# Optimization experiments

Hardware: AMD Instinct MI355X
Metric: run time of the kernel (lower is better)

## Reference

```python
import jax, jax.numpy as jnp
import numpy as np

N = 50000   # nodes
E = 800000  # edges (avg degree 16)
H = 128     # h_dim
S = 64      # s_dim
HID = 128   # master_selection_hidden_dim
K = 500     # num master nodes = master_rate(0.01) * N
LAM = 0.5   # lambda_attn


def setup_inputs() -> dict:
    key = jax.random.key(0)
    ks = jax.random.split(key, 24)
    rn = lambda k, shp, s: jax.random.normal(k, shp, dtype=jnp.float32) * s
    return {
        "h": rn(ks[0], (N, H), 1.0),
        "h_global": rn(ks[1], (N, H), 1.0),
        "pos": rn(ks[2], (N, 3), 1.0),
        "edge_index": jax.random.randint(ks[3], (2, E), 0, N, dtype=jnp.int32),
        "batch": jnp.zeros((N,), dtype=jnp.int32),
        "W_a": rn(ks[4], (H, H), H ** -0.5),
        "W_b": rn(ks[5], (H, H), H ** -0.5),
        "b1": rn(ks[6], (H,), 0.02),
        "W2": rn(ks[7], (H, H), H ** -0.5),
        "b2": rn(ks[8], (H,), 0.02),
        "W3": rn(ks[9], (2 * H, H), (2 * H) ** -0.5),
        "b3": rn(ks[10], (H,), 0.02),
        "w_virtual": jnp.float32(0.5),
        "Wm1": rn(ks[11], (S, HID), S ** -0.5),
        "bm1": rn(ks[12], (HID,), 0.02),
        "Wm2": rn(ks[13], (HID, 1), HID ** -0.5),
        "bm2": rn(ks[14], (1,), 0.02),
        "Wq": rn(ks[15], (S, S), S ** -0.5),
        "Wk": rn(ks[16], (S, S), S ** -0.5),
        "Wa1": rn(ks[17], (2 * H, H), (2 * H) ** -0.5),
        "ba1": rn(ks[18], (H,), 0.02),
        "Wa2": rn(ks[19], (H, H), H ** -0.5),
        "ba2": rn(ks[20], (H,), 0.02),
    }


def reference(h, h_global, pos, edge_index, batch, W_a, W_b, b1, W2, b2, W3, b3,
              w_virtual, Wm1, bm1, Wm2, bm2, Wq, Wk, Wa1, ba1, Wa2, ba2):
    n = h.shape[0]
    src, dst = edge_index[0], edge_index[1]

    def backbone_edges(x, p):
        # edge-list message passing: msg(src->dst) aggregated at dst
        a, bf = x @ W_a, x @ W_b
        d2 = jnp.sum((p[src] - p[dst]) ** 2, axis=-1)
        w = 1.0 / (1.0 + d2)  # distance decay
        msg = (jax.nn.silu(a[src] + bf[dst] + b1) @ W2 + b2) * w[:, None]
        agg = jax.ops.segment_sum(msg, dst, num_segments=n)
        return jnp.concatenate([x, agg], axis=-1) @ W3 + b3

    def backbone_dense(xm, pm, adj_w):
        # same message function over the dense K x K master graph; adj_w[i,j]
        # is the (possibly virtual-scaled) edge weight src=i -> dst=j
        a, bf = xm @ W_a, xm @ W_b
        d2 = jnp.sum((pm[:, None, :] - pm[None, :, :]) ** 2, axis=-1)
        w = adj_w / (1.0 + d2)
        msg = jax.nn.silu(a[:, None, :] + bf[None, :, :] + b1)  # [K, K, H]
        agg = jnp.einsum('ijh,ij->jh', msg, w) @ W2 + w.sum(0)[:, None] * b2
        return jnp.concatenate([xm, agg], axis=-1) @ W3 + b3

    # backbone update on full graph
    h_update = backbone_edges(h, pos)

    # master-node selection: learned score, top-K (static-shape stand-in
    # for the m > 0.5 dynamic mask; ratio-based selection as in MasterSelection)
    hs = h_global[:, :S]
    m = jax.nn.sigmoid((jax.nn.silu(hs @ Wm1 + bm1) @ Wm2 + bm2)[:, 0])  # [N]
    _, idx = jax.lax.top_k(m, K)
    is_master = jnp.zeros((n,), dtype=bool).at[idx].set(True)
    inv = jnp.zeros((n,), dtype=jnp.int32).at[idx].set(jnp.arange(K, dtype=jnp.int32))

    # induced dense adjacency over master nodes (subgraph + to_dense_adj)
    em = (is_master[src] & is_master[dst]).astype(jnp.float32)
    adj = jnp.zeros((K, K), dtype=jnp.float32).at[inv[src], inv[dst]].add(em)
    adj = (adj > 0).astype(jnp.float32)

    # virtual adjacency: scaled-dot attention blended with induced adjacency
    h_m, pos_m = h_global[idx], pos[idx]
    hms = h_m[:, :S]
    attn = jax.nn.softmax((hms @ Wq) @ (hms @ Wk).T / jnp.sqrt(jnp.float32(S)), axis=-1)
    blend = LAM * attn + (1.0 - LAM) * adj
    A_virtual = jnp.where(blend > 1.0 / K, blend, 0.0)

    # remove_self_loops + to_undirected on the virtual edge set (binary)
    eye = jnp.eye(K, dtype=bool)
    vadj = (A_virtual > 0) & ~eye
    vadj = (vadj | vadj.T).astype(jnp.float32)

    # hierarchical update over concatenated induced + virtual edges
    adj_w = adj + w_virtual * vadj
    h_master_update = backbone_dense(h_m, pos_m, adj_w)
    h_hier = h_m + h_master_update
    hexp = jnp.zeros_like(h_global).at[idx].set(h_hier)

    # gated attention fusion into h_global
    gate = jax.nn.silu(jnp.concatenate([h_global, hexp], axis=-1) @ Wa1 + ba1) @ Wa2 + ba2
    h_global_new = h_global + gate * hexp
    h_local = h + h_update
    return jnp.concatenate([h_local, h_global_new], axis=-1)  # [N, 2H]
```

## Files before the change

kernel.cpp:

```cpp
#include <hip/hip_runtime.h>
#include <math.h>

#define NN 50000
#define NE 800000
#define KS 500
#define NSL 8
#define SLICE 63

typedef unsigned short ushort_t;
typedef unsigned int uint_t;
typedef short bf16x8 __attribute__((ext_vector_type(8)));
typedef float f32x4 __attribute__((ext_vector_type(4)));

__device__ __forceinline__ float bf2f(ushort_t u) {
    return __uint_as_float(((uint_t)u) << 16);
}
__device__ __forceinline__ ushort_t f2bf(float f) {
    uint_t u = __float_as_uint(f);
    u += 0x7fffu + ((u >> 16) & 1u);
    return (ushort_t)(u >> 16);
}
__device__ __forceinline__ float fsilu(float x) {
    return x * __builtin_amdgcn_rcpf(1.f + __expf(-x));
}

__global__ __launch_bounds__(128) void prep_wt(
    const float* __restrict__ Wa, const float* __restrict__ Wb, const float* __restrict__ W3,
    ushort_t* __restrict__ Wta, ushort_t* __restrict__ Wtb, ushort_t* __restrict__ Wt3a)
{
    int j = blockIdx.x;
    int k = threadIdx.x;
    int y = blockIdx.y;
    const float* src = (y == 0) ? Wa : (y == 1) ? Wb : W3;
    ushort_t* dst = (y == 0) ? Wta : (y == 1) ? Wtb : Wt3a;
    dst[j * 128 + k] = f2bf(src[k * 128 + j]);
}

__global__ __launch_bounds__(128) void w23t_kernel(
    const float* __restrict__ W2, const float* __restrict__ W3, const float* __restrict__ b2,
    ushort_t* __restrict__ W23t, float* __restrict__ b23)
{
    int c = blockIdx.x;
    int j = threadIdx.x;
    if (c < 128) {
        float acc = 0.f;
        for (int k = 0; k < 128; ++k) acc = fmaf(W2[c * 128 + k], W3[(128 + k) * 128 + j], acc);
        W23t[j * 128 + c] = f2bf(acc);
    } else {
        float acc = 0.f;
        for (int k = 0; k < 128; ++k) acc = fmaf(b2[k], W3[(128 + k) * 128 + j], acc);
        b23[j] = acc;
    }
}

__global__ __launch_bounds__(512) void mfma_dual(
    const float* __restrict__ h, const ushort_t* __restrict__ Wta, const ushort_t* __restrict__ Wtb,
    ushort_t* __restrict__ C1, ushort_t* __restrict__ C2, int M)
{
    __shared__ ushort_t As[64][136];
    __shared__ ushort_t Wa_s[128][40];
    __shared__ ushort_t Wb_s[128][40];
    const int t = threadIdx.x;
    const int bm = blockIdx.x * 64;
    for (int idx = t * 4; idx < 64 * 128; idx += 2048) {
        int r = idx >> 7, c = idx & 127;
        int gr = bm + r;
        float4 v = make_float4(0.f, 0.f, 0.f, 0.f);
        if (gr < M) v = *(const float4*)(h + (size_t)gr * 128 + c);
        As[r][c + 0] = f2bf(v.x); As[r][c + 1] = f2bf(v.y);
        As[r][c + 2] = f2bf(v.z); As[r][c + 3] = f2bf(v.w);
    }
    const int w = t >> 6;
    const int lane = t & 63;
    const int rowgrp = w >> 1;
    const int mat = w & 1;
    const int i = lane & 15, g = lane >> 4;
    const int row = rowgrp * 16 + i;
    const ushort_t* wsrc = (t < 256) ? Wta : Wtb;
    ushort_t* wdst0 = (t < 256) ? &Wa_s[0][0] : &Wb_s[0][0];
    const int tt = t & 255;
    const int wr = tt >> 1, wc = (tt & 1) * 16;

    f32x4 acc[8];
#pragma unroll
    for (int n = 0; n < 8; ++n) acc[n] = (f32x4)0.f;

#pragma unroll
    for (int kk = 0; kk < 4; ++kk) {
        __syncthreads();
        {
            uint4 v0 = *(const uint4*)(wsrc + (size_t)wr * 128 + kk * 32 + wc);
            uint4 v1 = *(const uint4*)(wsrc + (size_t)wr * 128 + kk * 32 + wc + 8);
            *(uint4*)(wdst0 + wr * 40 + wc) = v0;
            *(uint4*)(wdst0 + wr * 40 + wc + 8) = v1;
        }
        __syncthreads();
        const ushort_t* Ws = mat ? &Wb_s[0][0] : &Wa_s[0][0];
        bf16x8 af = *(const bf16x8*)(&As[row][kk * 32 + g * 8]);
#pragma unroll
        for (int n = 0; n < 8; ++n) {
            bf16x8 bf = *(const bf16x8*)(Ws + (n * 16 + i) * 40 + g * 8);
            acc[n] = __builtin_amdgcn_mfma_f32_16x16x32_bf16(af, bf, acc[n], 0, 0, 0);
        }
    }
    ushort_t* C = mat ? C2 : C1;
    const int R = bm + rowgrp * 16;
#pragma unroll
    for (int n = 0; n < 8; ++n) {
        int col = n * 16 + i;
#pragma unroll
        for (int v = 0; v < 4; ++v) {
            int orow = R + 4 * g + v;
            if (orow < M) C[(size_t)orow * 128 + col] = f2bf(acc[n][v]);
        }
    }
}

__global__ __launch_bounds__(512) void mfma_local_fused(
    const float* __restrict__ h, const ushort_t* __restrict__ u16,
    const ushort_t* __restrict__ Wt3a, const ushort_t* __restrict__ W23t,
    const float* __restrict__ b23, const float* __restrict__ b3,
    const float* __restrict__ cw, const float* __restrict__ h_global,
    float* __restrict__ out, int M)
{
    __shared__ ushort_t Hs[64][136];
    __shared__ ushort_t Us[64][136];
    __shared__ ushort_t W3s[128][40];
    __shared__ ushort_t W2s[128][40];
    const int t = threadIdx.x;
    const int bm = blockIdx.x * 64;
    for (int idx = t * 4; idx < 64 * 128; idx += 2048) {
        int r = idx >> 7, c = idx & 127;
        int gr = bm + r;
        float4 v = make_float4(0.f, 0.f, 0.f, 0.f);
        uint2 uv = make_uint2(0, 0);
        if (gr < M) {
            v = *(const float4*)(h + (size_t)gr * 128 + c);
            uv = *(const uint2*)(u16 + (size_t)gr * 128 + c);
            float4 hgv = *(const float4*)(h_global + (size_t)gr * 128 + c);
            *(float4*)(out + (size_t)gr * 256 + 128 + c) = hgv;
        }
        Hs[r][c + 0] = f2bf(v.x); Hs[r][c + 1] = f2bf(v.y);
        Hs[r][c + 2] = f2bf(v.z); Hs[r][c + 3] = f2bf(v.w);
        Us[r][c + 0] = (ushort_t)(uv.x & 0xffff); Us[r][c + 1] = (ushort_t)(uv.x >> 16);
        Us[r][c + 2] = (ushort_t)(uv.y & 0xffff); Us[r][c + 3] = (ushort_t)(uv.y >> 16);
    }
    const int w = t >> 6;
    const int lane = t & 63;
    const int rowgrp = w >> 1;
    const int nb = (w & 1) * 4;
    const int i = lane & 15, g = lane >> 4;
    const int row = rowgrp * 16 + i;
    const ushort_t* wsrc = (t < 256) ? Wt3a : W23t;
    ushort_t* wdst0 = (t < 256) ? &W3s[0][0] : &W2s[0][0];
    const int tt = t & 255;
    const int wr = tt >> 1, wc = (tt & 1) * 16;

    f32x4 acc[4];
#pragma unroll
    for (int n = 0; n < 4; ++n) acc[n] = (f32x4)0.f;

#pragma unroll
    for (int kk = 0; kk < 4; ++kk) {
        __syncthreads();
        {
            uint4 v0 = *(const uint4*)(wsrc + (size_t)wr * 128 + kk * 32 + wc);
            uint4 v1 = *(const uint4*)(wsrc + (size_t)wr * 128 + kk * 32 + wc + 8);
            *(uint4*)(wdst0 + wr * 40 + wc) = v0;
            *(uint4*)(wdst0 + wr * 40 + wc + 8) = v1;
        }
        __syncthreads();
        bf16x8 aH = *(const bf16x8*)(&Hs[row][kk * 32 + g * 8]);
        bf16x8 aU = *(const bf16x8*)(&Us[row][kk * 32 + g * 8]);
#pragma unroll
        for (int n = 0; n < 4; ++n) {
            bf16x8 b3f = *(const bf16x8*)(&W3s[(nb + n) * 16 + i][g * 8]);
            bf16x8 b2f = *(const bf16x8*)(&W2s[(nb + n) * 16 + i][g * 8]);
            acc[n] = __builtin_amdgcn_mfma_f32_16x16x32_bf16(aH, b3f, acc[n], 0, 0, 0);
            acc[n] = __builtin_amdgcn_mfma_f32_16x16x32_bf16(aU, b2f, acc[n], 0, 0, 0);
        }
    }
    const int R = bm + rowgrp * 16;
    float cwv[4];
#pragma unroll
    for (int v = 0; v < 4; ++v) {
        int orow = R + 4 * g + v;
        cwv[v] = (orow < M) ? cw[orow] : 0.f;
    }
#pragma unroll
    for (int n = 0; n < 4; ++n) {
        int col = (nb + n) * 16 + i;
        float b3v = b3[col];
        float b23v = b23[col];
#pragma unroll
        for (int v = 0; v < 4; ++v) {
            int orow = R + 4 * g + v;
            if (orow < M) {
                float res = bf2f(Hs[rowgrp * 16 + 4 * g + v][col]);
                out[(size_t)orow * 256 + col] = acc[n][v] + b3v + cwv[v] * b23v + res;
            }
        }
    }
}

__global__ __launch_bounds__(256) void score_fused(
    const float* __restrict__ h_global, const float* __restrict__ Wm1,
    const float* __restrict__ bm1, const float* __restrict__ Wm2,
    const float* __restrict__ bm2, float* __restrict__ mout)
{
    __shared__ float Hs[64][64];
    const int t = threadIdx.x;
    const int bm = blockIdx.x * 64;
    for (int idx = t * 4; idx < 64 * 64; idx += 1024) {
        int r = idx >> 6, c = idx & 63;
        int gr = bm + r;
        float4 v = make_float4(0.f, 0.f, 0.f, 0.f);
        if (gr < NN) v = *(const float4*)(h_global + (size_t)gr * 128 + c);
        *(float4*)(&Hs[r][c]) = v;
    }
    __syncthreads();
    const int col = (t & 31) * 4;
    const int r0 = (t >> 5) * 8;
    float4 bmv = *(const float4*)(bm1 + col);
    float4 acc[8];
#pragma unroll
    for (int r = 0; r < 8; ++r) acc[r] = bmv;
    for (int k = 0; k < 64; ++k) {
        float4 w = *(const float4*)(Wm1 + k * 128 + col);
#pragma unroll
        for (int r = 0; r < 8; ++r) {
            float av = Hs[r0 + r][k];
            acc[r].x = fmaf(av, w.x, acc[r].x);
            acc[r].y = fmaf(av, w.y, acc[r].y);
            acc[r].z = fmaf(av, w.z, acc[r].z);
            acc[r].w = fmaf(av, w.w, acc[r].w);
        }
    }
    float4 w2v = *(const float4*)(Wm2 + col);
    float pr[8];
#pragma unroll
    for (int r = 0; r < 8; ++r) {
        float s = 0.f;
        s = fmaf(acc[r].x / (1.f + expf(-acc[r].x)), w2v.x, s);
        s = fmaf(acc[r].y / (1.f + expf(-acc[r].y)), w2v.y, s);
        s = fmaf(acc[r].z / (1.f + expf(-acc[r].z)), w2v.z, s);
        s = fmaf(acc[r].w / (1.f + expf(-acc[r].w)), w2v.w, s);
        pr[r] = s;
    }
#pragma unroll
    for (int off = 1; off < 32; off <<= 1) {
#pragma unroll
        for (int r = 0; r < 8; ++r) pr[r] += __shfl_xor(pr[r], off, 64);
    }
    if ((t & 31) == 0) {
        float bm2v = bm2[0];
#pragma unroll
        for (int r = 0; r < 8; ++r) {
            int gr = bm + r0 + r;
            if (gr < NN) mout[gr] = 1.f / (1.f + expf(-(pr[r] + bm2v)));
        }
    }
}

__global__ __launch_bounds__(256) void gemm_dual(
    const float* __restrict__ A, const float* __restrict__ W1, const float* __restrict__ W2,
    float* __restrict__ C1, float* __restrict__ C2, int M, int ldc)
{
    __shared__ float As[64][128];
    const int t = threadIdx.x;
    const int bm = blockIdx.x * 64;
    for (int idx = t * 4; idx < 64 * 128; idx += 1024) {
        int r = idx >> 7, c = idx & 127;
        int gr = bm + r;
        float4 v = make_float4(0.f, 0.f, 0.f, 0.f);
        if (gr < M) v = *(const float4*)(A + (size_t)gr * 128 + c);
        *(float4*)(&As[r][c]) = v;
    }
    __syncthreads();
    const int col = (t & 31) * 4;
    const int r0 = (t >> 5) * 8;
    float4 acc1[8], acc2[8];
#pragma unroll
    for (int r = 0; r < 8; ++r) { acc1[r] = make_float4(0,0,0,0); acc2[r] = make_float4(0,0,0,0); }
    for (int k = 0; k < 128; ++k) {
        float4 w1 = *(const float4*)(W1 + k * 128 + col);
        float4 w2 = *(const float4*)(W2 + k * 128 + col);
#pragma unroll
        for (int r = 0; r < 8; ++r) {
            float av = As[r0 + r][k];
            acc1[r].x = fmaf(av, w1.x, acc1[r].x);
            acc1[r].y = fmaf(av, w1.y, acc1[r].y);
            acc1[r].z = fmaf(av, w1.z, acc1[r].z);
            acc1[r].w = fmaf(av, w1.w, acc1[r].w);
            acc2[r].x = fmaf(av, w2.x, acc2[r].x);
            acc2[r].y = fmaf(av, w2.y, acc2[r].y);
            acc2[r].z = fmaf(av, w2.z, acc2[r].z);
            acc2[r].w = fmaf(av, w2.w, acc2[r].w);
        }
    }
#pragma unroll
    for (int r = 0; r < 8; ++r) {
        int gr = bm + r0 + r;
        if (gr < M) {
            *(float4*)(C1 + (size_t)gr * ldc + col) = acc1[r];
            *(float4*)(C2 + (size_t)gr * ldc + col) = acc2[r];
        }
    }
}

__global__ __launch_bounds__(256) void hist_pass(const float* __restrict__ m, int* state, int level)
{
    __shared__ int lh[256];
    lh[threadIdx.x] = 0;
    __syncthreads();
    int i = blockIdx.x * 256 + threadIdx.x;
    if (i == 0 && level == 0) state[257] = KS;
    if (i < NN) {
        unsigned v = __float_as_uint(m[i]);
        unsigned prefix = (unsigned)state[256];
        int shift = 32 - 8 * level;
        bool ok = (level == 0) || ((v >> shift) == prefix);
        if (ok) {
            unsigned byte = (v >> (shift - 8)) & 255u;
            atomicAdd(&lh[byte], 1);
        }
    }
    __syncthreads();
    if (lh[threadIdx.x]) atomicAdd(&state[threadIdx.x], lh[threadIdx.x]);
}

__global__ void hist_scan(int* state)
{
    int remaining = state[257];
    int cum = 0, bin = 0;
    for (int b = 255; b >= 0; --b) {
        int c = state[b];
        if (cum + c >= remaining) { bin = b; remaining -= cum; break; }
        cum += c;
    }
    state[256] = (int)(((unsigned)state[256] << 8) | (unsigned)bin);
    state[257] = remaining;
    for (int b = 0; b < 256; ++b) state[b] = 0;
}

__global__ __launch_bounds__(256) void select_topk(const float* __restrict__ m, int* state,
                                                   int* sel, int* tie_buf)
{
    int i = blockIdx.x * 256 + threadIdx.x;
    if (i >= NN) return;
    unsigned v = __float_as_uint(m[i]);
    unsigned T = (unsigned)state[256];
    if (v > T) {
        int p = atomicAdd(&state[258], 1);
        sel[p] = i;
    } else if (v == T) {
        int p = atomicAdd(&state[259], 1);
        if (p < 4096) tie_buf[p] = i;
    }
}

__global__ __launch_bounds__(256) void tie_resolve(int* state, int* sel, const int* tie_buf)
{
    int need = state[257];
    int cgt = state[258];
    int tcount = state[259];
    if (tcount > 4096) tcount = 4096;
    for (int t = threadIdx.x; t < tcount; t += blockDim.x) {
        int id = tie_buf[t];
        int rank = 0;
        for (int u = 0; u < tcount; ++u) rank += (tie_buf[u] < id);
        if (rank < need) sel[cgt + rank] = id;
    }
}

__global__ __launch_bounds__(128) void build_master(
    const int* __restrict__ sel, const float* __restrict__ h_global,
    const float* __restrict__ pos, int* __restrict__ is_master, int* __restrict__ inv,
    float* __restrict__ h_m, float* __restrict__ pos_m)
{
    int r = blockIdx.x;
    int t = threadIdx.x;
    int node = sel[r];
    if (t == 0) {
        is_master[node] = 1;
        inv[node] = r;
        pos_m[r * 3 + 0] = pos[(size_t)node * 3 + 0];
        pos_m[r * 3 + 1] = pos[(size_t)node * 3 + 1];
        pos_m[r * 3 + 2] = pos[(size_t)node * 3 + 2];
    }
    h_m[(size_t)r * 128 + t] = h_global[(size_t)node * 128 + t];
}

__global__ __launch_bounds__(256) void deg_hist(const int* __restrict__ ei, int* __restrict__ deg,
                                                int* __restrict__ rank)
{
    int e = blockIdx.x * 256 + threadIdx.x;
    if (e < NE) rank[e] = atomicAdd(&deg[ei[NE + e]], 1);
}

__global__ __launch_bounds__(256) void scan_part(const int* __restrict__ deg, int* __restrict__ part)
{
    __shared__ int red[256];
    int i = blockIdx.x * 256 + threadIdx.x;
    red[threadIdx.x] = (i < NN) ? deg[i] : 0;
    __syncthreads();
    for (int off = 128; off > 0; off >>= 1) {
        if (threadIdx.x < off) red[threadIdx.x] += red[threadIdx.x + off];
        __syncthreads();
    }
    if (threadIdx.x == 0) part[blockIdx.x] = red[0];
}

__global__ void scan_top(int* part, int np)
{
    if (threadIdx.x == 0) {
        int run = 0;
        for (int i = 0; i < np; ++i) { int v = part[i]; part[i] = run; run += v; }
    }
}

__global__ __launch_bounds__(256) void scan_final(const int* __restrict__ deg, const int* __restrict__ part,
                                                  int* __restrict__ offs)
{
    __shared__ int sh[256];
    int i = blockIdx.x * 256 + threadIdx.x;
    int v = (i < NN) ? deg[i] : 0;
    sh[threadIdx.x] = v;
    __syncthreads();
    for (int off = 1; off < 256; off <<= 1) {
        int add = (threadIdx.x >= off) ? sh[threadIdx.x - off] : 0;
        __syncthreads();
        sh[threadIdx.x] += add;
        __syncthreads();
    }
    int excl = sh[threadIdx.x] - v + part[blockIdx.x];
    if (i < NN) offs[i] = excl;
}

__global__ __launch_bounds__(256) void edge_scatter_adj(
    const int* __restrict__ ei, const float* __restrict__ pos,
    const int* __restrict__ offs, const int* __restrict__ rank,
    const int* __restrict__ is_master, const int* __restrict__ inv,
    int2* __restrict__ eslot, int* __restrict__ adj_i)
{
    int e = blockIdx.x * 256 + threadIdx.x;
    if (e >= NE) return;
    int s = ei[e];
    int d = ei[NE + e];
    float dx = pos[(size_t)s * 3 + 0] - pos[(size_t)d * 3 + 0];
    float dy = pos[(size_t)s * 3 + 1] - pos[(size_t)d * 3 + 1];
    float dz = pos[(size_t)s * 3 + 2] - pos[(size_t)d * 3 + 2];
    float w = 1.f / (1.f + dx * dx + dy * dy + dz * dz);
    eslot[offs[d] + rank[e]] = make_int2(s, __float_as_int(w));
    if (is_master[s] && is_master[d]) atomicOr(&adj_i[inv[s] * KS + inv[d]], 1);
}

__global__ __launch_bounds__(256) void edge_agg(
    const int2* __restrict__ eslot, const int* __restrict__ offs, const int* __restrict__ deg,
    const ushort_t* __restrict__ a16, const ushort_t* __restrict__ b16,
    const float* __restrict__ b1, ushort_t* __restrict__ u16, float* __restrict__ cw)
{
    int wid = (blockIdx.x * 256 + threadIdx.x) >> 6;
    int lane = threadIdx.x & 63;
    if (wid >= NN) return;
    int off = offs[wid];
    int n = deg[wid];
    float2 b1v = *(const float2*)(b1 + 2 * lane);
    uint_t bw = ((const uint_t*)(b16 + (size_t)wid * 128))[lane];
    float bf0 = bf2f((ushort_t)(bw & 0xffff)) + b1v.x;
    float bf1 = bf2f((ushort_t)(bw >> 16)) + b1v.y;
    float acc0 = 0.f, acc1 = 0.f, cwa = 0.f;
    int k = 0;
    for (; k + 4 <= n; k += 4) {
        int2 e0 = eslot[off + k];
        int2 e1 = eslot[off + k + 1];
        int2 e2 = eslot[off + k + 2];
        int2 e3 = eslot[off + k + 3];
        uint_t aw0 = ((const uint_t*)(a16 + (size_t)e0.x * 128))[lane];
        uint_t aw1 = ((const uint_t*)(a16 + (size_t)e1.x * 128))[lane];
        uint_t aw2 = ((const uint_t*)(a16 + (size_t)e2.x * 128))[lane];
        uint_t aw3 = ((const uint_t*)(a16 + (size_t)e3.x * 128))[lane];
        float w0 = __int_as_float(e0.y), w1 = __int_as_float(e1.y);
        float w2 = __int_as_float(e2.y), w3 = __int_as_float(e3.y);
        acc0 = fmaf(fsilu(bf2f((ushort_t)(aw0 & 0xffff)) + bf0), w0, acc0);
        acc1 = fmaf(fsilu(bf2f((ushort_t)(aw0 >> 16)) + bf1), w0, acc1);
        acc0 = fmaf(fsilu(bf2f((ushort_t)(aw1 & 0xffff)) + bf0), w1, acc0);
        acc1 = fmaf(fsilu(bf2f((ushort_t)(aw1 >> 16)) + bf1), w1, acc1);
        acc0 = fmaf(fsilu(bf2f((ushort_t)(aw2 & 0xffff)) + bf0), w2, acc0);
        acc1 = fmaf(fsilu(bf2f((ushort_t)(aw2 >> 16)) + bf1), w2, acc1);
        acc0 = fmaf(fsilu(bf2f((ushort_t)(aw3 & 0xffff)) + bf0), w3, acc0);
        acc1 = fmaf(fsilu(bf2f((ushort_t)(aw3 >> 16)) + bf1), w3, acc1);
        cwa += w0 + w1 + w2 + w3;
    }
    for (; k < n; ++k) {
        int2 e0 = eslot[off + k];
        uint_t aw0 = ((const uint_t*)(a16 + (size_t)e0.x * 128))[lane];
        float w0 = __int_as_float(e0.y);
        acc0 = fmaf(fsilu(bf2f((ushort_t)(aw0 & 0xffff)) + bf0), w0, acc0);
        acc1 = fmaf(fsilu(bf2f((ushort_t)(aw0 >> 16)) + bf1), w0, acc1);
        cwa += w0;
    }
    uint_t packed = (uint_t)f2bf(acc0) | ((uint_t)f2bf(acc1) << 16);
    ((uint_t*)(u16 + (size_t)wid * 128))[lane] = packed;
    if (lane == 0) cw[wid] = cwa;
}

__global__ __launch_bounds__(64) void qk_proj(
    const float* __restrict__ h_m, const float* __restrict__ Wq, const float* __restrict__ Wk,
    float* __restrict__ q, float* __restrict__ kk)
{
    int r = blockIdx.x;
    int t = threadIdx.x;
    __shared__ float hs[64];
    hs[t] = h_m[(size_t)r * 128 + t];
    __syncthreads();
    float aq = 0.f, ak = 0.f;
    for (int s = 0; s < 64; ++s) {
        float hv = hs[s];
        aq = fmaf(hv, Wq[s * 64 + t], aq);
        ak = fmaf(hv, Wk[s * 64 + t], ak);
    }
    q[r * 64 + t] = aq;
    kk[r * 64 + t] = ak;
}

__global__ __launch_bounds__(512) void attn_blend(
    const float* __restrict__ q, const float* __restrict__ kk,
    const int* __restrict__ adj_i, int* __restrict__ B)
{
    int i = blockIdx.x;
    int t = threadIdx.x;
    __shared__ float qi[64];
    __shared__ float red[512];
    if (t < 64) qi[t] = q[i * 64 + t];
    __syncthreads();
    float s = -1e30f;
    if (t < KS) {
        float acc = 0.f;
        for (int c = 0; c < 64; ++c) acc = fmaf(qi[c], kk[t * 64 + c], acc);
        s = acc * 0.125f;
    }
    red[t] = s;
    __syncthreads();
    for (int off = 256; off > 0; off >>= 1) {
        if (t < off) red[t] = fmaxf(red[t], red[t + off]);
        __syncthreads();
    }
    float mx = red[0];
    __syncthreads();
    float e = (t < KS) ? expf(s - mx) : 0.f;
    red[t] = e;
    __syncthreads();
    for (int off = 256; off > 0; off >>= 1) {
        if (t < off) red[t] += red[t + off];
        __syncthreads();
    }
    float denom = red[0];
    if (t < KS) {
        float attn = e / denom;
        float blend = 0.5f * attn + 0.5f * (adj_i[i * KS + t] ? 1.f : 0.f);
        B[i * KS + t] = (blend > (1.f / (float)KS)) && (t != i);
    }
}

__global__ __launch_bounds__(256) void wmat_kernel(
    const int* __restrict__ adj_i, const int* __restrict__ B,
    const float* __restrict__ w_virtual, const float* __restrict__ pos_m,
    float* __restrict__ wT)
{
    int idx = blockIdx.x * 256 + threadIdx.x;
    if (idx >= KS * KS) return;
    int j = idx / KS, i = idx % KS;
    int ij = i * KS + j;
    float adjf = adj_i[ij] ? 1.f : 0.f;
    float v = (B[ij] | B[j * KS + i]) ? 1.f : 0.f;
    float aw = adjf + w_virtual[0] * v;
    float dx = pos_m[i * 3 + 0] - pos_m[j * 3 + 0];
    float dy = pos_m[i * 3 + 1] - pos_m[j * 3 + 1];
    float dz = pos_m[i * 3 + 2] - pos_m[j * 3 + 2];
    wT[idx] = aw / (1.f + dx * dx + dy * dy + dz * dz);
}

__global__ __launch_bounds__(64) void cwm_kernel(const float* __restrict__ wT, float* __restrict__ cw_m)
{
    int j = blockIdx.x;
    int lane = threadIdx.x;
    float s = 0.f;
    for (int i = lane; i < KS; i += 64) s += wT[j * KS + i];
    for (int off = 32; off > 0; off >>= 1) s += __shfl_down(s, off);
    if (lane == 0) cw_m[j] = s;
}

__global__ __launch_bounds__(128) void dense_agg(
    const float* __restrict__ a_m, const float* __restrict__ bf_m,
    const float* __restrict__ b1, const float* __restrict__ wT,
    float* __restrict__ partial)
{
    int j = blockIdx.x;
    int sl = blockIdx.y;
    int t = threadIdx.x;
    int i0 = sl * SLICE;
    int i1 = min(KS, i0 + SLICE);
    float bfj = bf_m[(size_t)j * 128 + t] + b1[t];
    float acc = 0.f;
    for (int i = i0; i < i1; ++i) {
        float w = wT[j * KS + i];
        float x = a_m[(size_t)i * 128 + t] + bfj;
        acc = fmaf(fsilu(x), w, acc);
    }
    partial[((size_t)sl * KS + j) * 128 + t] = acc;
}

__global__ __launch_bounds__(128) void master_update(
    const float* __restrict__ h_m, const float* __restrict__ partial, const float* __restrict__ cw_m,
    const float* __restrict__ W2, const float* __restrict__ b2,
    const float* __restrict__ W3, const float* __restrict__ b3, float* __restrict__ h_hier)
{
    int j = blockIdx.x;
    int t = threadIdx.x;
    __shared__ float tsh[128], hsh[128], ash[128];
    float tv = 0.f;
#pragma unroll
    for (int sl = 0; sl < NSL; ++sl) tv += partial[((size_t)sl * KS + j) * 128 + t];
    tsh[t] = tv;
    hsh[t] = h_m[(size_t)j * 128 + t];
    __syncthreads();
    float acc = cw_m[j] * b2[t];
    for (int c = 0; c < 128; ++c) acc = fmaf(tsh[c], W2[c * 128 + t], acc);
    ash[t] = acc;
    __syncthreads();
    float upd = b3[t];
    for (int c = 0; c < 128; ++c) upd = fmaf(hsh[c], W3[c * 128 + t], upd);
    for (int c = 0; c < 128; ++c) upd = fmaf(ash[c], W3[(128 + c) * 128 + t], upd);
    h_hier[(size_t)j * 128 + t] = hsh[t] + upd;
}

__global__ __launch_bounds__(128) void gate_kernel(
    const int* __restrict__ sel, const float* __restrict__ h_global,
    const float* __restrict__ h_hier, const float* __restrict__ Wa1,
    const float* __restrict__ ba1, const float* __restrict__ Wa2,
    const float* __restrict__ ba2, float* __restrict__ out)
{
    int j = blockIdx.x;
    int t = threadIdx.x;
    int node = sel[j];
    __shared__ float x[256];
    __shared__ float g1[128];
    x[t] = h_global[(size_t)node * 128 + t];
    x[128 + t] = h_hier[(size_t)j * 128 + t];
    __syncthreads();
    float acc = ba1[t];
    for (int c = 0; c < 256; ++c) acc = fmaf(x[c], Wa1[c * 128 + t], acc);
    g1[t] = acc / (1.f + expf(-acc));
    __syncthreads();
    float g = ba2[t];
    for (int c = 0; c < 128; ++c) g = fmaf(g1[c], Wa2[c * 128 + t], g);
    out[(size_t)node * 256 + 128 + t] = x[t] + g * x[128 + t];
}

extern "C" void kernel_launch(void* const* d_in, const int* in_sizes, int n_in,
                              void* d_out, int out_size, void* d_ws, size_t ws_size,
                              hipStream_t stream)
{
    const float* h        = (const float*)d_in[0];
    const float* h_global = (const float*)d_in[1];
    const float* pos      = (const float*)d_in[2];
    const int*   ei       = (const int*)d_in[3];
    const float* W_a      = (const float*)d_in[5];
    const float* W_b      = (const float*)d_in[6];
    const float* b1       = (const float*)d_in[7];
    const float* W2       = (const float*)d_in[8];
    const float* b2       = (const float*)d_in[9];
    const float* W3       = (const float*)d_in[10];
    const float* b3       = (const float*)d_in[11];
    const float* w_virt   = (const float*)d_in[12];
    const float* Wm1      = (const float*)d_in[13];
    const float* bm1      = (const float*)d_in[14];
    const float* Wm2      = (const float*)d_in[15];
    const float* bm2      = (const float*)d_in[16];
    const float* Wq       = (const float*)d_in[17];
    const float* Wk       = (const float*)d_in[18];
    const float* Wa1      = (const float*)d_in[19];
    const float* ba1      = (const float*)d_in[20];
    const float* Wa2      = (const float*)d_in[21];
    const float* ba2      = (const float*)d_in[22];
    float* out = (float*)d_out;

    char* p = (char*)d_ws;
    auto alloc = [&](size_t bytes) -> void* {
        void* q = (void*)p;
        p += (bytes + 255) & ~(size_t)255;
        return q;
    };
    ushort_t* u16   = (ushort_t*)alloc((size_t)NN * 128 * 2);
    float* mscore   = (float*)alloc((size_t)NN * 4);
    float* cw       = (float*)alloc((size_t)NN * 4);
    int*   is_mast  = (int*)alloc((size_t)NN * 4);
    int*   inv      = (int*)alloc((size_t)NN * 4);
    int*   deg      = (int*)alloc((size_t)NN * 4);
    int*   offs     = (int*)alloc((size_t)NN * 4);
    int*   rank     = (int*)alloc((size_t)NE * 4);
    int2*  eslot    = (int2*)alloc((size_t)NE * 8);
    int*   part     = (int*)alloc(256 * 4);
    int*   sel      = (int*)alloc((size_t)KS * 4);
    float* h_m      = (float*)alloc((size_t)KS * 128 * 4);
    float* pos_m    = (float*)alloc((size_t)KS * 3 * 4);
    float* qm       = (float*)alloc((size_t)KS * 64 * 4);
    float* km       = (float*)alloc((size_t)KS * 64 * 4);
    int*   adj_i    = (int*)alloc((size_t)KS * KS * 4);
    int*   Bmat     = (int*)alloc((size_t)KS * KS * 4);
    float* wT       = (float*)alloc((size_t)KS * KS * 4);
    float* a_m      = (float*)alloc((size_t)KS * 128 * 4);
    float* bf_m     = (float*)alloc((size_t)KS * 128 * 4);
    float* partial  = (float*)alloc((size_t)NSL * KS * 128 * 4);
    float* cw_m     = (float*)alloc((size_t)KS * 4);
    float* h_hier   = (float*)alloc((size_t)KS * 128 * 4);
    ushort_t* Wta   = (ushort_t*)alloc(128 * 128 * 2);
    ushort_t* Wtb   = (ushort_t*)alloc(128 * 128 * 2);
    ushort_t* Wt3a  = (ushort_t*)alloc(128 * 128 * 2);
    ushort_t* W23t  = (ushort_t*)alloc(128 * 128 * 2);
    float* b23      = (float*)alloc(128 * 4);
    int*   state    = (int*)alloc(1024 * 4);
    int*   tie_buf  = (int*)alloc(4096 * 4);

    ushort_t* a16 = (ushort_t*)out;
    ushort_t* b16 = a16 + (size_t)NN * 128;

    hipMemsetAsync(deg, 0, (size_t)NN * 4, stream);
    hipMemsetAsync(is_mast, 0, (size_t)NN * 4, stream);
    hipMemsetAsync(adj_i, 0, (size_t)KS * KS * 4, stream);
    hipMemsetAsync(state, 0, 1024 * 4, stream);

    const int gemmN64 = (NN + 63) / 64;
    const int gemmK = (KS + 63) / 64;
    const int g196 = (NN + 255) / 256;
    const int gE   = (NE + 255) / 256;

    prep_wt<<<dim3(128, 3), 128, 0, stream>>>(W_a, W_b, W3, Wta, Wtb, Wt3a);
    w23t_kernel<<<129, 128, 0, stream>>>(W2, W3, b2, W23t, b23);

    mfma_dual<<<gemmN64, 512, 0, stream>>>(h, Wta, Wtb, a16, b16, NN);

    deg_hist<<<gE, 256, 0, stream>>>(ei, deg, rank);
    scan_part<<<g196, 256, 0, stream>>>(deg, part);
    scan_top<<<1, 64, 0, stream>>>(part, g196);
    scan_final<<<g196, 256, 0, stream>>>(deg, part, offs);

    score_fused<<<gemmN64, 256, 0, stream>>>(h_global, Wm1, bm1, Wm2, bm2, mscore);
    for (int lvl = 0; lvl < 4; ++lvl) {
        hist_pass<<<g196, 256, 0, stream>>>(mscore, state, lvl);
        hist_scan<<<1, 1, 0, stream>>>(state);
    }
    select_topk<<<g196, 256, 0, stream>>>(mscore, state, sel, tie_buf);
    tie_resolve<<<1, 256, 0, stream>>>(state, sel, tie_buf);
    build_master<<<KS, 128, 0, stream>>>(sel, h_global, pos, is_mast, inv, h_m, pos_m);

    edge_scatter_adj<<<gE, 256, 0, stream>>>(ei, pos, offs, rank, is_mast, inv, eslot, adj_i);

    edge_agg<<<(NN * 64) / 256, 256, 0, stream>>>(eslot, offs, deg, a16, b16, b1, u16, cw);

    qk_proj<<<KS, 64, 0, stream>>>(h_m, Wq, Wk, qm, km);
    attn_blend<<<KS, 512, 0, stream>>>(qm, km, adj_i, Bmat);

    wmat_kernel<<<(KS * KS + 255) / 256, 256, 0, stream>>>(adj_i, Bmat, w_virt, pos_m, wT);
    cwm_kernel<<<KS, 64, 0, stream>>>(wT, cw_m);

    gemm_dual<<<gemmK, 256, 0, stream>>>(h_m, W_a, W_b, a_m, bf_m, KS, 128);
    dense_agg<<<dim3(KS, NSL), 128, 0, stream>>>(a_m, bf_m, b1, wT, partial);
    master_update<<<KS, 128, 0, stream>>>(h_m, partial, cw_m, W2, b2, W3, b3, h_hier);

    mfma_local_fused<<<gemmN64, 512, 0, stream>>>(h, u16, Wt3a, W23t, b23, b3, cw,
                                                  h_global, out, NN);

    gate_kernel<<<KS, 128, 0, stream>>>(sel, h_global, h_hier, Wa1, ba1, Wa2, ba2, out);
}
```

Baseline: 363.0 us.

## Fuse scan/topk launches via last-block pattern and pack edge slots to 32 bits

Merges histogram-scan, select/tie-resolve and partial-scan kernels using a last-block-done atomic counter, so the serial steps run in the final block instead of separate launches. Groups the zeroed buffers contiguously so one memset replaces four. Packs each edge slot as a 16-bit source index plus a bf16 distance weight, halving CSR slot traffic in the edge aggregation. This trades weight precision for bandwidth and depends on the node count fitting in 16 bits.

```diff
diff --git a/kernel.cpp b/kernel.cpp
--- a/kernel.cpp
+++ b/kernel.cpp
@@ -308,68 +308,78 @@
     }
 }
 
-__global__ __launch_bounds__(256) void hist_pass(const float* __restrict__ m, int* state, int level)
+__global__ __launch_bounds__(256) void hist_fused(const float* __restrict__ m, int* state, int level)
 {
     __shared__ int lh[256];
+    __shared__ int amLast;
     lh[threadIdx.x] = 0;
+    if (threadIdx.x == 0) amLast = 0;
     __syncthreads();
     int i = blockIdx.x * 256 + threadIdx.x;
-    if (i == 0 && level == 0) state[257] = KS;
     if (i < NN) {
         unsigned v = __float_as_uint(m[i]);
-        unsigned prefix = (unsigned)state[256];
         int shift = 32 - 8 * level;
-        bool ok = (level == 0) || ((v >> shift) == prefix);
-        if (ok) {
-            unsigned byte = (v >> (shift - 8)) & 255u;
-            atomicAdd(&lh[byte], 1);
-        }
+        bool ok = (level == 0) || ((v >> shift) == (unsigned)state[256]);
+        if (ok) atomicAdd(&lh[(v >> (shift - 8)) & 255u], 1);
     }
     __syncthreads();
     if (lh[threadIdx.x]) atomicAdd(&state[threadIdx.x], lh[threadIdx.x]);
-}
-
-__global__ void hist_scan(int* state)
-{
-    int remaining = state[257];
-    int cum = 0, bin = 0;
-    for (int b = 255; b >= 0; --b) {
-        int c = state[b];
-        if (cum + c >= remaining) { bin = b; remaining -= cum; break; }
-        cum += c;
-    }
-    state[256] = (int)(((unsigned)state[256] << 8) | (unsigned)bin);
-    state[257] = remaining;
-    for (int b = 0; b < 256; ++b) state[b] = 0;
-}
-
-__global__ __launch_bounds__(256) void select_topk(const float* __restrict__ m, int* state,
-                                                   int* sel, int* tie_buf)
-{
+    __threadfence();
+    __syncthreads();
+    if (threadIdx.x == 0) {
+        if (atomicAdd(&state[260 + level], 1) == (int)gridDim.x - 1) amLast = 1;
+    }
+    __syncthreads();
+    if (amLast && threadIdx.x == 0) {
+        __threadfence();
+        int remaining = (level == 0) ? KS : state[257];
+        int cum = 0, bin = 0;
+        for (int b = 255; b >= 0; --b) {
+            int c = state[b];
+            if (cum + c >= remaining) { bin = b; remaining -= cum; break; }
+            cum += c;
+        }
+        state[256] = (level == 0) ? bin : (int)(((unsigned)state[256] << 8) | (unsigned)bin);
+        state[257] = remaining;
+        for (int b = 0; b < 256; ++b) state[b] = 0;
+    }
+}
+
+__global__ __launch_bounds__(256) void select_fused(const float* __restrict__ m, int* state,
+                                                    int* sel, int* tie_buf)
+{
+    __shared__ int amLast;
+    if (threadIdx.x == 0) amLast = 0;
+    __syncthreads();
     int i = blockIdx.x * 256 + threadIdx.x;
-    if (i >= NN) return;
-    unsigned v = __float_as_uint(m[i]);
-    unsigned T = (unsigned)state[256];
-    if (v > T) {
-        int p = atomicAdd(&state[258], 1);
-        sel[p] = i;
-    } else if (v == T) {
-        int p = atomicAdd(&state[259], 1);
-        if (p < 4096) tie_buf[p] = i;
-    }
-}
-
-__global__ __launch_bounds__(256) void tie_resolve(int* state, int* sel, const int* tie_buf)
-{
-    int need = state[257];
-    int cgt = state[258];
-    int tcount = state[259];
-    if (tcount > 4096) tcount = 4096;
-    for (int t = threadIdx.x; t < tcount; t += blockDim.x) {
-        int id = tie_buf[t];
-        int rank = 0;
-        for (int u = 0; u < tcount; ++u) rank += (tie_buf[u] < id);
-        if (rank < need) sel[cgt + rank] = id;
+    if (i < NN) {
+        unsigned v = __float_as_uint(m[i]);
+        unsigned T = (unsigned)state[256];
+        if (v > T) {
+            sel[atomicAdd(&state[258], 1)] = i;
+        } else if (v == T) {
+            int p = atomicAdd(&state[259], 1);
+            if (p < 4096) tie_buf[p] = i;
+        }
+    }
+    __threadfence();
+    __syncthreads();
+    if (threadIdx.x == 0) {
+        if (atomicAdd(&state[265], 1) == (int)gridDim.x - 1) amLast = 1;
+    }
+    __syncthreads();
+    if (amLast) {
+        __threadfence();
+        int need = state[257];
+        int cgt = state[258];
+        int tcount = state[259];
+        if (tcount > 4096) tcount = 4096;
+        for (int t2 = threadIdx.x; t2 < tcount; t2 += 256) {
+            int id = tie_buf[t2];
+            int rk = 0;
+            for (int u = 0; u < tcount; ++u) rk += (tie_buf[u] < id);
+            if (rk < need) sel[cgt + rk] = id;
+        }
     }
 }
 
@@ -398,9 +408,12 @@
     if (e < NE) rank[e] = atomicAdd(&deg[ei[NE + e]], 1);
 }
 
-__global__ __launch_bounds__(256) void scan_part(const int* __restrict__ deg, int* __restrict__ part)
+__global__ __launch_bounds__(256) void scan_part_fused(const int* __restrict__ deg,
+                                                       int* __restrict__ part, int* state)
 {
     __shared__ int red[256];
+    __shared__ int amLast;
+    if (threadIdx.x == 0) amLast = 0;
     int i = blockIdx.x * 256 + threadIdx.x;
     red[threadIdx.x] = (i < NN) ? deg[i] : 0;
     __syncthreads();
@@ -409,13 +422,16 @@
         __syncthreads();
     }
     if (threadIdx.x == 0) part[blockIdx.x] = red[0];
-}
-
-__global__ void scan_top(int* part, int np)
-{
+    __threadfence();
+    __syncthreads();
     if (threadIdx.x == 0) {
+        if (atomicAdd(&state[264], 1) == (int)gridDim.x - 1) amLast = 1;
+    }
+    __syncthreads();
+    if (amLast && threadIdx.x == 0) {
+        __threadfence();
         int run = 0;
-        for (int i = 0; i < np; ++i) { int v = part[i]; part[i] = run; run += v; }
+        for (int b = 0; b < (int)gridDim.x; ++b) { int v = part[b]; part[b] = run; run += v; }
     }
 }
 
@@ -441,7 +457,7 @@
     const int* __restrict__ ei, const float* __restrict__ pos,
     const int* __restrict__ offs, const int* __restrict__ rank,
     const int* __restrict__ is_master, const int* __restrict__ inv,
-    int2* __restrict__ eslot, int* __restrict__ adj_i)
+    uint_t* __restrict__ eslot, int* __restrict__ adj_i)
 {
     int e = blockIdx.x * 256 + threadIdx.x;
     if (e >= NE) return;
@@ -451,12 +467,12 @@
     float dy = pos[(size_t)s * 3 + 1] - pos[(size_t)d * 3 + 1];
     float dz = pos[(size_t)s * 3 + 2] - pos[(size_t)d * 3 + 2];
     float w = 1.f / (1.f + dx * dx + dy * dy + dz * dz);
-    eslot[offs[d] + rank[e]] = make_int2(s, __float_as_int(w));
+    eslot[offs[d] + rank[e]] = (uint_t)s | ((uint_t)f2bf(w) << 16);
     if (is_master[s] && is_master[d]) atomicOr(&adj_i[inv[s] * KS + inv[d]], 1);
 }
 
 __global__ __launch_bounds__(256) void edge_agg(
-    const int2* __restrict__ eslot, const int* __restrict__ offs, const int* __restrict__ deg,
+    const uint_t* __restrict__ eslot, const int* __restrict__ offs, const int* __restrict__ deg,
     const ushort_t* __restrict__ a16, const ushort_t* __restrict__ b16,
     const float* __restrict__ b1, ushort_t* __restrict__ u16, float* __restrict__ cw)
 {
@@ -472,16 +488,16 @@
     float acc0 = 0.f, acc1 = 0.f, cwa = 0.f;
     int k = 0;
     for (; k + 4 <= n; k += 4) {
-        int2 e0 = eslot[off + k];
-        int2 e1 = eslot[off + k + 1];
-        int2 e2 = eslot[off + k + 2];
-        int2 e3 = eslot[off + k + 3];
-        uint_t aw0 = ((const uint_t*)(a16 + (size_t)e0.x * 128))[lane];
-        uint_t aw1 = ((const uint_t*)(a16 + (size_t)e1.x * 128))[lane];
-        uint_t aw2 = ((const uint_t*)(a16 + (size_t)e2.x * 128))[lane];
-        uint_t aw3 = ((const uint_t*)(a16 + (size_t)e3.x * 128))[lane];
-        float w0 = __int_as_float(e0.y), w1 = __int_as_float(e1.y);
-        float w2 = __int_as_float(e2.y), w3 = __int_as_float(e3.y);
+        uint_t e0 = eslot[off + k];
+        uint_t e1 = eslot[off + k + 1];
+        uint_t e2 = eslot[off + k + 2];
+        uint_t e3 = eslot[off + k + 3];
+        uint_t aw0 = ((const uint_t*)(a16 + (size_t)(e0 & 0xffff) * 128))[lane];
+        uint_t aw1 = ((const uint_t*)(a16 + (size_t)(e1 & 0xffff) * 128))[lane];
+        uint_t aw2 = ((const uint_t*)(a16 + (size_t)(e2 & 0xffff) * 128))[lane];
+        uint_t aw3 = ((const uint_t*)(a16 + (size_t)(e3 & 0xffff) * 128))[lane];
+        float w0 = bf2f((ushort_t)(e0 >> 16)), w1 = bf2f((ushort_t)(e1 >> 16));
+        float w2 = bf2f((ushort_t)(e2 >> 16)), w3 = bf2f((ushort_t)(e3 >> 16));
         acc0 = fmaf(fsilu(bf2f((ushort_t)(aw0 & 0xffff)) + bf0), w0, acc0);
         acc1 = fmaf(fsilu(bf2f((ushort_t)(aw0 >> 16)) + bf1), w0, acc1);
         acc0 = fmaf(fsilu(bf2f((ushort_t)(aw1 & 0xffff)) + bf0), w1, acc0);
@@ -493,9 +509,9 @@
         cwa += w0 + w1 + w2 + w3;
     }
     for (; k < n; ++k) {
-        int2 e0 = eslot[off + k];
-        uint_t aw0 = ((const uint_t*)(a16 + (size_t)e0.x * 128))[lane];
-        float w0 = __int_as_float(e0.y);
+        uint_t e0 = eslot[off + k];
+        uint_t aw0 = ((const uint_t*)(a16 + (size_t)(e0 & 0xffff) * 128))[lane];
+        float w0 = bf2f((ushort_t)(e0 >> 16));
         acc0 = fmaf(fsilu(bf2f((ushort_t)(aw0 & 0xffff)) + bf0), w0, acc0);
         acc1 = fmaf(fsilu(bf2f((ushort_t)(aw0 >> 16)) + bf1), w0, acc1);
         cwa += w0;
@@ -692,22 +708,26 @@
         p += (bytes + 255) & ~(size_t)255;
         return q;
     };
+    int*   deg      = (int*)alloc((size_t)NN * 4);
+    int*   is_mast  = (int*)alloc((size_t)NN * 4);
+    int*   adj_i    = (int*)alloc((size_t)KS * KS * 4);
+    int*   state    = (int*)alloc(1024 * 4);
+    char*  zero_end = p;
+    size_t zero_bytes = (size_t)(zero_end - (char*)deg);
+
     ushort_t* u16   = (ushort_t*)alloc((size_t)NN * 128 * 2);
     float* mscore   = (float*)alloc((size_t)NN * 4);
     float* cw       = (float*)alloc((size_t)NN * 4);
-    int*   is_mast  = (int*)alloc((size_t)NN * 4);
     int*   inv      = (int*)alloc((size_t)NN * 4);
-    int*   deg      = (int*)alloc((size_t)NN * 4);
     int*   offs     = (int*)alloc((size_t)NN * 4);
     int*   rank     = (int*)alloc((size_t)NE * 4);
-    int2*  eslot    = (int2*)alloc((size_t)NE * 8);
+    uint_t* eslot   = (uint_t*)alloc((size_t)NE * 4);
     int*   part     = (int*)alloc(256 * 4);
     int*   sel      = (int*)alloc((size_t)KS * 4);
     float* h_m      = (float*)alloc((size_t)KS * 128 * 4);
     float* pos_m    = (float*)alloc((size_t)KS * 3 * 4);
     float* qm       = (float*)alloc((size_t)KS * 64 * 4);
     float* km       = (float*)alloc((size_t)KS * 64 * 4);
-    int*   adj_i    = (int*)alloc((size_t)KS * KS * 4);
     int*   Bmat     = (int*)alloc((size_t)KS * KS * 4);
     float* wT       = (float*)alloc((size_t)KS * KS * 4);
     float* a_m      = (float*)alloc((size_t)KS * 128 * 4);
@@ -720,16 +740,12 @@
     ushort_t* Wt3a  = (ushort_t*)alloc(128 * 128 * 2);
     ushort_t* W23t  = (ushort_t*)alloc(128 * 128 * 2);
     float* b23      = (float*)alloc(128 * 4);
-    int*   state    = (int*)alloc(1024 * 4);
     int*   tie_buf  = (int*)alloc(4096 * 4);
 
     ushort_t* a16 = (ushort_t*)out;
     ushort_t* b16 = a16 + (size_t)NN * 128;
 
-    hipMemsetAsync(deg, 0, (size_t)NN * 4, stream);
-    hipMemsetAsync(is_mast, 0, (size_t)NN * 4, stream);
-    hipMemsetAsync(adj_i, 0, (size_t)KS * KS * 4, stream);
-    hipMemsetAsync(state, 0, 1024 * 4, stream);
+    hipMemsetAsync(deg, 0, zero_bytes, stream);
 
     const int gemmN64 = (NN + 63) / 64;
     const int gemmK = (KS + 63) / 64;
@@ -742,17 +758,13 @@
     mfma_dual<<<gemmN64, 512, 0, stream>>>(h, Wta, Wtb, a16, b16, NN);
 
     deg_hist<<<gE, 256, 0, stream>>>(ei, deg, rank);
-    scan_part<<<g196, 256, 0, stream>>>(deg, part);
-    scan_top<<<1, 64, 0, stream>>>(part, g196);
+    scan_part_fused<<<g196, 256, 0, stream>>>(deg, part, state);
     scan_final<<<g196, 256, 0, stream>>>(deg, part, offs);
 
     score_fused<<<gemmN64, 256, 0, stream>>>(h_global, Wm1, bm1, Wm2, bm2, mscore);
-    for (int lvl = 0; lvl < 4; ++lvl) {
-        hist_pass<<<g196, 256, 0, stream>>>(mscore, state, lvl);
-        hist_scan<<<1, 1, 0, stream>>>(state);
-    }
-    select_topk<<<g196, 256, 0, stream>>>(mscore, state, sel, tie_buf);
-    tie_resolve<<<1, 256, 0, stream>>>(state, sel, tie_buf);
+    for (int lvl = 0; lvl < 4; ++lvl)
+        hist_fused<<<g196, 256, 0, stream>>>(mscore, state, lvl);
+    select_fused<<<g196, 256, 0, stream>>>(mscore, state, sel, tie_buf);
     build_master<<<KS, 128, 0, stream>>>(sel, h_global, pos, is_mast, inv, h_m, pos_m);
 
     edge_scatter_adj<<<gE, 256, 0, stream>>>(ei, pos, offs, rank, is_mast, inv, eslot, adj_i);
```

After: 435.4 us. 20.0% more time.

## Pack edge slots into 32-bit index+bf16 weight and merge memsets

Applied to the files above, without the earlier changes.

Edge slots now store the 16-bit source index and a bf16 distance weight in one 32-bit word instead of an int2. This halves the eslot write and read traffic in the scatter and aggregation kernels. The zero-initialized buffers are placed next to each other so a single memset clears all of them. The weight precision drops to bf16, and the packing relies on the node count fitting in 16 bits.

```diff
diff --git a/kernel.cpp b/kernel.cpp
--- a/kernel.cpp
+++ b/kernel.cpp
@@ -441,7 +441,7 @@
     const int* __restrict__ ei, const float* __restrict__ pos,
     const int* __restrict__ offs, const int* __restrict__ rank,
     const int* __restrict__ is_master, const int* __restrict__ inv,
-    int2* __restrict__ eslot, int* __restrict__ adj_i)
+    uint_t* __restrict__ eslot, int* __restrict__ adj_i)
 {
     int e = blockIdx.x * 256 + threadIdx.x;
     if (e >= NE) return;
@@ -451,12 +451,12 @@
     float dy = pos[(size_t)s * 3 + 1] - pos[(size_t)d * 3 + 1];
     float dz = pos[(size_t)s * 3 + 2] - pos[(size_t)d * 3 + 2];
     float w = 1.f / (1.f + dx * dx + dy * dy + dz * dz);
-    eslot[offs[d] + rank[e]] = make_int2(s, __float_as_int(w));
+    eslot[offs[d] + rank[e]] = (uint_t)s | ((uint_t)f2bf(w) << 16);
     if (is_master[s] && is_master[d]) atomicOr(&adj_i[inv[s] * KS + inv[d]], 1);
 }
 
 __global__ __launch_bounds__(256) void edge_agg(
-    const int2* __restrict__ eslot, const int* __restrict__ offs, const int* __restrict__ deg,
+    const uint_t* __restrict__ eslot, const int* __restrict__ offs, const int* __restrict__ deg,
     const ushort_t* __restrict__ a16, const ushort_t* __restrict__ b16,
     const float* __restrict__ b1, ushort_t* __restrict__ u16, float* __restrict__ cw)
 {
@@ -472,16 +472,16 @@
     float acc0 = 0.f, acc1 = 0.f, cwa = 0.f;
     int k = 0;
     for (; k + 4 <= n; k += 4) {
-        int2 e0 = eslot[off + k];
-        int2 e1 = eslot[off + k + 1];
-        int2 e2 = eslot[off + k + 2];
-        int2 e3 = eslot[off + k + 3];
-        uint_t aw0 = ((const uint_t*)(a16 + (size_t)e0.x * 128))[lane];
-        uint_t aw1 = ((const uint_t*)(a16 + (size_t)e1.x * 128))[lane];
-        uint_t aw2 = ((const uint_t*)(a16 + (size_t)e2.x * 128))[lane];
-        uint_t aw3 = ((const uint_t*)(a16 + (size_t)e3.x * 128))[lane];
-        float w0 = __int_as_float(e0.y), w1 = __int_as_float(e1.y);
-        float w2 = __int_as_float(e2.y), w3 = __int_as_float(e3.y);
+        uint_t e0 = eslot[off + k];
+        uint_t e1 = eslot[off + k + 1];
+        uint_t e2 = eslot[off + k + 2];
+        uint_t e3 = eslot[off + k + 3];
+        uint_t aw0 = ((const uint_t*)(a16 + (size_t)(e0 & 0xffff) * 128))[lane];
+        uint_t aw1 = ((const uint_t*)(a16 + (size_t)(e1 & 0xffff) * 128))[lane];
+        uint_t aw2 = ((const uint_t*)(a16 + (size_t)(e2 & 0xffff) * 128))[lane];
+        uint_t aw3 = ((const uint_t*)(a16 + (size_t)(e3 & 0xffff) * 128))[lane];
+        float w0 = bf2f((ushort_t)(e0 >> 16)), w1 = bf2f((ushort_t)(e1 >> 16));
+        float w2 = bf2f((ushort_t)(e2 >> 16)), w3 = bf2f((ushort_t)(e3 >> 16));
         acc0 = fmaf(fsilu(bf2f((ushort_t)(aw0 & 0xffff)) + bf0), w0, acc0);
         acc1 = fmaf(fsilu(bf2f((ushort_t)(aw0 >> 16)) + bf1), w0, acc1);
         acc0 = fmaf(fsilu(bf2f((ushort_t)(aw1 & 0xffff)) + bf0), w1, acc0);
@@ -493,9 +493,9 @@
         cwa += w0 + w1 + w2 + w3;
     }
     for (; k < n; ++k) {
-        int2 e0 = eslot[off + k];
-        uint_t aw0 = ((const uint_t*)(a16 + (size_t)e0.x * 128))[lane];
-        float w0 = __int_as_float(e0.y);
+        uint_t e0 = eslot[off + k];
+        uint_t aw0 = ((const uint_t*)(a16 + (size_t)(e0 & 0xffff) * 128))[lane];
+        float w0 = bf2f((ushort_t)(e0 >> 16));
         acc0 = fmaf(fsilu(bf2f((ushort_t)(aw0 & 0xffff)) + bf0), w0, acc0);
         acc1 = fmaf(fsilu(bf2f((ushort_t)(aw0 >> 16)) + bf1), w0, acc1);
         cwa += w0;
@@ -692,22 +692,26 @@
         p += (bytes + 255) & ~(size_t)255;
         return q;
     };
+    int*   deg      = (int*)alloc((size_t)NN * 4);
+    int*   is_mast  = (int*)alloc((size_t)NN * 4);
+    int*   adj_i    = (int*)alloc((size_t)KS * KS * 4);
+    int*   state    = (int*)alloc(1024 * 4);
+    char*  zero_end = p;
+    size_t zero_bytes = (size_t)(zero_end - (char*)deg);
+
     ushort_t* u16   = (ushort_t*)alloc((size_t)NN * 128 * 2);
     float* mscore   = (float*)alloc((size_t)NN * 4);
     float* cw       = (float*)alloc((size_t)NN * 4);
-    int*   is_mast  = (int*)alloc((size_t)NN * 4);
     int*   inv      = (int*)alloc((size_t)NN * 4);
-    int*   deg      = (int*)alloc((size_t)NN * 4);
     int*   offs     = (int*)alloc((size_t)NN * 4);
     int*   rank     = (int*)alloc((size_t)NE * 4);
-    int2*  eslot    = (int2*)alloc((size_t)NE * 8);
+    uint_t* eslot   = (uint_t*)alloc((size_t)NE * 4);
     int*   part     = (int*)alloc(256 * 4);
     int*   sel      = (int*)alloc((size_t)KS * 4);
     float* h_m      = (float*)alloc((size_t)KS * 128 * 4);
     float* pos_m    = (float*)alloc((size_t)KS * 3 * 4);
     float* qm       = (float*)alloc((size_t)KS * 64 * 4);
     float* km       = (float*)alloc((size_t)KS * 64 * 4);
-    int*   adj_i    = (int*)alloc((size_t)KS * KS * 4);
     int*   Bmat     = (int*)alloc((size_t)KS * KS * 4);
     float* wT       = (float*)alloc((size_t)KS * KS * 4);
     float* a_m      = (float*)alloc((size_t)KS * 128 * 4);
@@ -720,16 +724,12 @@
     ushort_t* Wt3a  = (ushort_t*)alloc(128 * 128 * 2);
     ushort_t* W23t  = (ushort_t*)alloc(128 * 128 * 2);
     float* b23      = (float*)alloc(128 * 4);
-    int*   state    = (int*)alloc(1024 * 4);
     int*   tie_buf  = (int*)alloc(4096 * 4);
 
     ushort_t* a16 = (ushort_t*)out;
     ushort_t* b16 = a16 + (size_t)NN * 128;
 
-    hipMemsetAsync(deg, 0, (size_t)NN * 4, stream);
-    hipMemsetAsync(is_mast, 0, (size_t)NN * 4, stream);
-    hipMemsetAsync(adj_i, 0, (size_t)KS * KS * 4, stream);
-    hipMemsetAsync(state, 0, 1024 * 4, stream);
+    hipMemsetAsync(deg, 0, zero_bytes, stream);
 
     const int gemmN64 = (NN + 63) / 64;
     const int gemmK = (KS + 63) / 64;
```

Measured after the change: 357.9 us. About the same (-1.4%).
